# Optimization experiments

Hardware: AMD Instinct MI355X
Metric: run time of the kernel (lower is better)

## Reference

```python
import jax, jax.numpy as jnp
import numpy as np

HARD_RATIO = 0.5
HARD_WEIGHT = 0.5
B, Q, D = 1024, 32, 512


def _l2norm(x):
    return x / jnp.linalg.norm(x, axis=-1, keepdims=True)


def setup_inputs() -> dict:
    key = jax.random.key(0)
    k1, k2 = jax.random.split(key)
    fusion_feats = _l2norm(jax.random.normal(k1, (B, D), dtype=jnp.float32))
    target_feats = _l2norm(jax.random.normal(k2, (B, Q, D), dtype=jnp.float32))
    temp = jnp.float32(0.07)
    return {"fusion_feats": fusion_feats, "target_feats": target_feats, "temp": temp}


def reference(fusion_feats, target_feats, temp):
    b = fusion_feats.shape[0]
    # sim[i, j, q] = fusion[i] . target[j, q]  -> max over query tokens q
    sim = jnp.einsum('id,jqd->ijq', fusion_feats, target_feats)  # (B, B, Q)
    sim_max = jnp.max(sim, axis=-1) / temp                        # (B, B)

    # standard InfoNCE with diagonal labels
    loss_standard = -jnp.mean(jnp.diagonal(jax.nn.log_softmax(sim_max, axis=-1)))

    # online hard-negative mining: per-row top-k over off-diagonal entries
    num_hard = max(1, int(b * HARD_RATIO))
    diag_mask = jnp.eye(b, dtype=bool)
    masked = jnp.where(diag_mask, -jnp.inf, sim_max)
    hard_sims, _ = jax.lax.top_k(masked, num_hard)                # (B, num_hard)
    pos = jnp.diagonal(sim_max)                                    # (B,)
    # -log(exp(pos) / (exp(pos) + sum exp(hard))) = logsumexp([pos, hard]) - pos
    lse = jax.nn.logsumexp(jnp.concatenate([pos[:, None], hard_sims], axis=1), axis=1)
    hard_loss_online = jnp.mean(lse - pos)

    total_loss = loss_standard + HARD_WEIGHT * hard_loss_online
    return total_loss
```

## Files before the change

### kernel.cpp

```cpp
#include <hip/hip_runtime.h>
#include <hip/hip_bf16.h>
#include <math.h>

typedef unsigned short u16;
typedef unsigned char u8;
typedef unsigned int u32;
typedef long long i64;
typedef __attribute__((ext_vector_type(4))) float f32x4;

__global__ void cvt_fused(const float* __restrict__ F, const float* __restrict__ T,
                          u32* __restrict__ Fb, u32* __restrict__ Tb,
                          float* __restrict__ out) {
    const int idx = blockIdx.x * blockDim.x + threadIdx.x;
    if (idx == 0) out[0] = 0.f;
    const float* s;
    u32* d;
    int i;
    if (idx < 65536) { s = F; d = Fb; i = idx; }
    else             { s = T; d = Tb; i = idx - 65536; }
    const float4 v0 = *(const float4*)(s + (size_t)i * 8);
    const float4 v1 = *(const float4*)(s + (size_t)i * 8 + 4);
    int lo = __builtin_amdgcn_cvt_pk_fp8_f32(v0.x * 16.f, v0.y * 16.f, 0, false);
    lo     = __builtin_amdgcn_cvt_pk_fp8_f32(v0.z * 16.f, v0.w * 16.f, lo, true);
    int hi = __builtin_amdgcn_cvt_pk_fp8_f32(v1.x * 16.f, v1.y * 16.f, 0, false);
    hi     = __builtin_amdgcn_cvt_pk_fp8_f32(v1.z * 16.f, v1.w * 16.f, hi, true);
    uint2 o; o.x = (u32)lo; o.y = (u32)hi;
    const int r  = i >> 6;
    const int ob = (i & 63) << 3;
    const int t  = ob >> 7;
    const int ss = (ob >> 5) & 3;
    const int f  = (ob >> 3) & 3;
    const int o2 = (t << 7) | (f << 5) | (ss << 3);
    ((uint2*)d)[r * 64 + (o2 >> 3)] = o;
}

#define GLB_AS __attribute__((address_space(1)))
#define LDS_AS __attribute__((address_space(3)))

__device__ __forceinline__ void gload_lds16(const void* g, void* l) {
    __builtin_amdgcn_global_load_lds((const GLB_AS void*)g, (LDS_AS void*)l, 16, 0, 0);
}

__device__ __forceinline__ i64 half0(int4 v) { int2 p; p.x = v.x; p.y = v.y; return __builtin_bit_cast(i64, p); }
__device__ __forceinline__ i64 half1(int4 v) { int2 p; p.x = v.z; p.y = v.w; return __builtin_bit_cast(i64, p); }

__global__ __launch_bounds__(256, 4)
void gemm_max(const u8* __restrict__ A, const u8* __restrict__ B,
              const float* __restrict__ temp_ptr, float* __restrict__ sim) {
    __shared__ __align__(16) u8 lA[64 * 128];
    __shared__ __align__(16) u8 lB[128 * 128];
    const int bn = blockIdx.x;
    const int bm = blockIdx.y;
    const int tid  = threadIdx.x;
    const int wave = tid >> 6;
    const int lane = tid & 63;
    const int wm = wave >> 1;
    const int wn = wave & 1;

    f32x4 acc[2][4] = {};

    const int srow = lane >> 3;
    const int aoff = srow * 512 + (((lane & 7) ^ srow) << 4);
    const u8* gA = A + (size_t)(bm * 64)  * 512 + aoff;
    const u8* gB = B + (size_t)(bn * 128) * 512 + aoff;

    const int frow = lane & 15;
    const int fq   = lane >> 4;
    const int r7   = frow & 7;

    for (int k0 = 0; k0 < 512; k0 += 128) {
        gload_lds16(gA + (wave)     * 4096 + k0, lA + (wave)     * 1024);
        gload_lds16(gA + (wave + 4) * 4096 + k0, lA + (wave + 4) * 1024);
#pragma unroll
        for (int j = 0; j < 4; ++j)
            gload_lds16(gB + (wave + 4 * j) * 4096 + k0, lB + (wave + 4 * j) * 1024);
        __syncthreads();

#pragma unroll
        for (int sp = 0; sp < 2; ++sp) {
            const int coff = (((fq << 1) + sp) ^ r7) << 4;
            int4 aF[2], bF[4];
#pragma unroll
            for (int mt = 0; mt < 2; ++mt)
                aF[mt] = *(const int4*)&lA[(wm * 32 + mt * 16 + frow) * 128 + coff];
#pragma unroll
            for (int nt = 0; nt < 4; ++nt)
                bF[nt] = *(const int4*)&lB[(wn * 64 + nt * 16 + frow) * 128 + coff];
#pragma unroll
            for (int mt = 0; mt < 2; ++mt)
#pragma unroll
                for (int nt = 0; nt < 4; ++nt) {
                    acc[mt][nt] = __builtin_amdgcn_mfma_f32_16x16x32_fp8_fp8(
                        half0(aF[mt]), half0(bF[nt]), acc[mt][nt], 0, 0, 0);
                    acc[mt][nt] = __builtin_amdgcn_mfma_f32_16x16x32_fp8_fp8(
                        half1(aF[mt]), half1(bF[nt]), acc[mt][nt], 0, 0, 0);
                }
        }
        __syncthreads();
    }

    const float inv = 1.0f / (256.0f * (*temp_ptr));
    const int jb = (bn * 128 + wn * 64) >> 5;
#pragma unroll
    for (int mt = 0; mt < 2; ++mt) {
#pragma unroll
        for (int rr = 0; rr < 4; ++rr) {
            float v0 = fmaxf(acc[mt][0][rr], acc[mt][1][rr]);
            float v1 = fmaxf(acc[mt][2][rr], acc[mt][3][rr]);
#pragma unroll
            for (int off = 1; off < 16; off <<= 1) {
                v0 = fmaxf(v0, __shfl_xor(v0, off));
                v1 = fmaxf(v1, __shfl_xor(v1, off));
            }
            if ((lane & 15) == 0) {
                const int row = bm * 64 + wm * 32 + mt * 16 + fq * 4 + rr;
                sim[row * 1024 + jb]     = v0 * inv;
                sim[row * 1024 + jb + 1] = v1 * inv;
            }
        }
    }
}

__device__ __forceinline__ u32 f2key(float x) {
    u32 b = __float_as_uint(x);
    return (b & 0x80000000u) ? ~b : (b | 0x80000000u);
}
__device__ __forceinline__ float key2f(u32 k) {
    return __uint_as_float((k & 0x80000000u) ? (k & 0x7fffffffu) : ~k);
}

__global__ __launch_bounds__(256)
void row_loss(const float* __restrict__ sim, float* __restrict__ out) {
    const int tid = threadIdx.x;
    const int lane = tid & 63;
    const int wv = tid >> 6;
    const int i = blockIdx.x * 4 + wv;

    float v[16];
    const float4* rp = (const float4*)(sim + (size_t)i * 1024);
#pragma unroll
    for (int t = 0; t < 4; ++t) {
        float4 f = rp[t * 64 + lane];
        v[t * 4 + 0] = f.x; v[t * 4 + 1] = f.y; v[t * 4 + 2] = f.z; v[t * 4 + 3] = f.w;
    }

    const int dslot = ((i >> 8) << 2) | (i & 3);
    const int dlane = (i >> 2) & 63;

    u32 k[16];
#pragma unroll
    for (int t = 0; t < 16; ++t) {
        u32 kk = f2key(v[t]);
        k[t] = (lane == dlane && t == dslot) ? 0u : kk;
    }

    float pv = 0.f;
#pragma unroll
    for (int t = 0; t < 16; ++t) if (t == dslot) pv = v[t];
    const float pos = __shfl(pv, dlane);

    float m = v[0];
#pragma unroll
    for (int t = 1; t < 16; ++t) m = fmaxf(m, v[t]);
#pragma unroll
    for (int off = 32; off > 0; off >>= 1) m = fmaxf(m, __shfl_xor(m, off));
    float s = 0.f;
#pragma unroll
    for (int t = 0; t < 16; ++t) s += __expf(v[t] - m);
#pragma unroll
    for (int off = 32; off > 0; off >>= 1) s += __shfl_xor(s, off);
    const float loss_std = m + __logf(s) - pos;

    u32 lo = 0u, hi = 0xFFFFFFFFu;
    while (lo < hi) {
        const u32 span = hi - lo;
        const u32 mid = lo + (span >> 1) + (span & 1u);
        int cnt = 0;
#pragma unroll
        for (int t = 0; t < 16; ++t) cnt += (k[t] >= mid);
#pragma unroll
        for (int off = 32; off > 0; off >>= 1) cnt += __shfl_xor(cnt, off);
        if (cnt >= 512) lo = mid; else hi = mid - 1;
    }
    const u32 t_key = lo;
    const float tval = key2f(t_key);

    float se = 0.f;
    int cgt = 0;
#pragma unroll
    for (int t = 0; t < 16; ++t) {
        if (k[t] > t_key) { se += __expf(v[t] - m); ++cgt; }
    }
#pragma unroll
    for (int off = 32; off > 0; off >>= 1) se += __shfl_xor(se, off);
#pragma unroll
    for (int off = 32; off > 0; off >>= 1) cgt += __shfl_xor(cgt, off);

    const float sh = se + (float)(512 - cgt) * __expf(tval - m) + __expf(pos - m);
    const float hard = m + __logf(sh) - pos;

    if (lane == 0)
        atomicAdd(out, (loss_std + 0.5f * hard) * (1.0f / 1024.0f));
}

extern "C" void kernel_launch(void* const* d_in, const int* in_sizes, int n_in,
                              void* d_out, int out_size, void* d_ws, size_t ws_size,
                              hipStream_t stream) {
    const float* F    = (const float*)d_in[0];
    const float* T    = (const float*)d_in[1];
    const float* temp = (const float*)d_in[2];
    float* out = (float*)d_out;

    char* ws = (char*)d_ws;
    u32*  Fb8 = (u32*)ws;
    u32*  Tb8 = (u32*)(ws + (1u << 20));
    float* sim = (float*)(ws + (1u << 20) + (32u << 20));

    cvt_fused<<<8448, 256, 0, stream>>>(F, T, Fb8, Tb8, out);

    dim3 grid(256, 16);
    gemm_max<<<grid, 256, 0, stream>>>((const u8*)Fb8, (const u8*)Tb8, temp, sim);

    row_loss<<<256, 256, 0, stream>>>(sim, out);
}
```

Baseline: 158.2 us.

## Switch to 32x32x16 fp8 MFMA with 128x128 block tiles and new layout

Replaces the 16x16x32 fp8 MFMA with the 32x32x16 variant, enlarges the A tile from 64 to 128 rows so each block computes a 128x128 tile, and halves the grid in M. The fp8 conversion kernel permutes the K layout to match the new fragment loads, and the epilogue reduces the max over 32-lane groups per output register. The goal is higher MFMA throughput per instruction and more reuse of B per load, at the cost of more LDS per block and a heavier shuffle epilogue. The conversion store also contains a stray extra write before the real store.

```diff
diff --git a/kernel.cpp b/kernel.cpp
--- a/kernel.cpp
+++ b/kernel.cpp
@@ -6,7 +6,7 @@
 typedef unsigned char u8;
 typedef unsigned int u32;
 typedef long long i64;
-typedef __attribute__((ext_vector_type(4))) float f32x4;
+typedef __attribute__((ext_vector_type(16))) float f32x16;
 
 __global__ void cvt_fused(const float* __restrict__ F, const float* __restrict__ T,
                           u32* __restrict__ Fb, u32* __restrict__ Tb,
@@ -26,12 +26,11 @@
     hi     = __builtin_amdgcn_cvt_pk_fp8_f32(v1.z * 16.f, v1.w * 16.f, hi, true);
     uint2 o; o.x = (u32)lo; o.y = (u32)hi;
     const int r  = i >> 6;
-    const int ob = (i & 63) << 3;
-    const int t  = ob >> 7;
-    const int ss = (ob >> 5) & 3;
-    const int f  = (ob >> 3) & 3;
-    const int o2 = (t << 7) | (f << 5) | (ss << 3);
-    ((uint2*)d)[r * 64 + (o2 >> 3)] = o;
+    const int l6 = i & 63;
+    const int t  = (l6 >> 4) & 3;
+    const int ss = (l6 >> 1) & 7;
+    const int h  = l6 & 1;
+    d[(r << 6) + (t << 4) + (h << 3) + ss] = 0, ((uint2*)d)[(r << 6) + (t << 4) + (h << 3) + ss] = o;
 }
 
 #define GLB_AS __attribute__((address_space(1)))
@@ -47,7 +46,7 @@
 __global__ __launch_bounds__(256, 4)
 void gemm_max(const u8* __restrict__ A, const u8* __restrict__ B,
               const float* __restrict__ temp_ptr, float* __restrict__ sim) {
-    __shared__ __align__(16) u8 lA[64 * 128];
+    __shared__ __align__(16) u8 lA[128 * 128];
     __shared__ __align__(16) u8 lB[128 * 128];
     const int bn = blockIdx.x;
     const int bm = blockIdx.y;
@@ -57,42 +56,43 @@
     const int wm = wave >> 1;
     const int wn = wave & 1;
 
-    f32x4 acc[2][4] = {};
+    f32x16 acc[2][2] = {};
 
     const int srow = lane >> 3;
     const int aoff = srow * 512 + (((lane & 7) ^ srow) << 4);
-    const u8* gA = A + (size_t)(bm * 64)  * 512 + aoff;
+    const u8* gA = A + (size_t)(bm * 128) * 512 + aoff;
     const u8* gB = B + (size_t)(bn * 128) * 512 + aoff;
 
-    const int frow = lane & 15;
-    const int fq   = lane >> 4;
-    const int r7   = frow & 7;
+    const int l31 = lane & 31;
+    const int h   = lane >> 5;
+    const int r7  = l31 & 7;
+    const int gquad = l31 >> 3;
 
     for (int k0 = 0; k0 < 512; k0 += 128) {
-        gload_lds16(gA + (wave)     * 4096 + k0, lA + (wave)     * 1024);
-        gload_lds16(gA + (wave + 4) * 4096 + k0, lA + (wave + 4) * 1024);
-#pragma unroll
-        for (int j = 0; j < 4; ++j)
+#pragma unroll
+        for (int j = 0; j < 4; ++j) {
+            gload_lds16(gA + (wave + 4 * j) * 4096 + k0, lA + (wave + 4 * j) * 1024);
             gload_lds16(gB + (wave + 4 * j) * 4096 + k0, lB + (wave + 4 * j) * 1024);
+        }
         __syncthreads();
 
 #pragma unroll
-        for (int sp = 0; sp < 2; ++sp) {
-            const int coff = (((fq << 1) + sp) ^ r7) << 4;
-            int4 aF[2], bF[4];
+        for (int t = 0; t < 4; ++t) {
+            const int csw = ((((h << 2) + t) ^ r7) << 4) + (r7 << 7);
+            int4 aF[2], bF[2];
 #pragma unroll
             for (int mt = 0; mt < 2; ++mt)
-                aF[mt] = *(const int4*)&lA[(wm * 32 + mt * 16 + frow) * 128 + coff];
-#pragma unroll
-            for (int nt = 0; nt < 4; ++nt)
-                bF[nt] = *(const int4*)&lB[(wn * 64 + nt * 16 + frow) * 128 + coff];
+                aF[mt] = *(const int4*)&lA[((wm * 8 + mt * 4 + gquad) << 10) + csw];
+#pragma unroll
+            for (int nt = 0; nt < 2; ++nt)
+                bF[nt] = *(const int4*)&lB[((wn * 8 + nt * 4 + gquad) << 10) + csw];
 #pragma unroll
             for (int mt = 0; mt < 2; ++mt)
 #pragma unroll
-                for (int nt = 0; nt < 4; ++nt) {
-                    acc[mt][nt] = __builtin_amdgcn_mfma_f32_16x16x32_fp8_fp8(
+                for (int nt = 0; nt < 2; ++nt) {
+                    acc[mt][nt] = __builtin_amdgcn_mfma_f32_32x32x16_fp8_fp8(
                         half0(aF[mt]), half0(bF[nt]), acc[mt][nt], 0, 0, 0);
-                    acc[mt][nt] = __builtin_amdgcn_mfma_f32_16x16x32_fp8_fp8(
+                    acc[mt][nt] = __builtin_amdgcn_mfma_f32_32x32x16_fp8_fp8(
                         half1(aF[mt]), half1(bF[nt]), acc[mt][nt], 0, 0, 0);
                 }
         }
@@ -100,22 +100,22 @@
     }
 
     const float inv = 1.0f / (256.0f * (*temp_ptr));
-    const int jb = (bn * 128 + wn * 64) >> 5;
 #pragma unroll
     for (int mt = 0; mt < 2; ++mt) {
 #pragma unroll
-        for (int rr = 0; rr < 4; ++rr) {
-            float v0 = fmaxf(acc[mt][0][rr], acc[mt][1][rr]);
-            float v1 = fmaxf(acc[mt][2][rr], acc[mt][3][rr]);
-#pragma unroll
-            for (int off = 1; off < 16; off <<= 1) {
-                v0 = fmaxf(v0, __shfl_xor(v0, off));
-                v1 = fmaxf(v1, __shfl_xor(v1, off));
-            }
-            if ((lane & 15) == 0) {
-                const int row = bm * 64 + wm * 32 + mt * 16 + fq * 4 + rr;
-                sim[row * 1024 + jb]     = v0 * inv;
-                sim[row * 1024 + jb + 1] = v1 * inv;
+        for (int nt = 0; nt < 2; ++nt) {
+            const int j = bn * 4 + wn * 2 + nt;
+#pragma unroll
+            for (int reg = 0; reg < 16; ++reg) {
+                float v = acc[mt][nt][reg];
+#pragma unroll
+                for (int off = 1; off <= 16; off <<= 1)
+                    v = fmaxf(v, __shfl_xor(v, off));
+                if (l31 == 0) {
+                    const int row = bm * 128 + wm * 64 + mt * 32
+                                  + (reg & 3) + 8 * (reg >> 2) + 4 * h;
+                    sim[row * 1024 + j] = v * inv;
+                }
             }
         }
     }
@@ -218,7 +218,7 @@
 
     cvt_fused<<<8448, 256, 0, stream>>>(F, T, Fb8, Tb8, out);
 
-    dim3 grid(256, 16);
+    dim3 grid(256, 8);
     gemm_max<<<grid, 256, 0, stream>>>((const u8*)Fb8, (const u8*)Tb8, temp, sim);
 
     row_loss<<<256, 256, 0, stream>>>(sim, out);
```

Result: slower. 174.5 us (+10.3%).
